# Kernel optimization log

Measured on AMD Instinct MI355X. Metric: run time of the kernel, lower is better.

## Reference

```python
import jax, jax.numpy as jnp
import numpy as np

N = 50000   # nodes
E = 400000  # edges
IN = 64     # input feature dim
H = 4       # heads (layers 1-2)
C = 128     # hidden channels per head
NEG_SLOPE = 0.2


def gat_conv(x, W, a_src, a_dst, b, src, dst, num_nodes):
    """PyG-style GATConv (add_self_loops=False, dropout inactive / eval mode).
    x: [N, F_in]; W: [F_in, H*C]; a_src/a_dst: [H, C]; b: [H*C].
    Returns concat-over-heads output [N, H*C]."""
    h = (x @ W).reshape(num_nodes, a_src.shape[0], a_src.shape[1])  # [N,H,C]
    alpha_s = jnp.einsum('nhc,hc->nh', h, a_src)  # [N,H]
    alpha_d = jnp.einsum('nhc,hc->nh', h, a_dst)  # [N,H]
    e = jax.nn.leaky_relu(alpha_s[src] + alpha_d[dst], NEG_SLOPE)  # [E,H]
    # numerically-stable segment softmax over incoming edges of each dst node
    m = jax.ops.segment_max(e, dst, num_segments=num_nodes)       # [N,H]
    m = jnp.where(jnp.isfinite(m), m, 0.0)                        # empty segments
    p = jnp.exp(e - m[dst])                                       # [E,H]
    denom = jax.ops.segment_sum(p, dst, num_segments=num_nodes)   # [N,H]
    alpha = p / (denom[dst] + 1e-16)                              # [E,H]
    # message = alpha * h[src], scatter-add into dst
    out = jax.ops.segment_sum(alpha[:, :, None] * h[src], dst,
                              num_segments=num_nodes)             # [N,H,C]
    return out.reshape(num_nodes, -1) + b


def setup_inputs() -> dict:
    key = jax.random.key(0)
    ks = jax.random.split(key, 16)
    s = 0.1  # weight scale for stability
    inp = {
        'x': jax.random.normal(ks[0], (N, IN), dtype=jnp.float32),
        'edge_index': jax.random.randint(ks[1], (2, E), 0, N, dtype=jnp.int64),
        # layer 1: 64 -> H*C
        'W1': s * jax.random.normal(ks[2], (IN, H * C), dtype=jnp.float32),
        'a_src1': s * jax.random.normal(ks[3], (H, C), dtype=jnp.float32),
        'a_dst1': s * jax.random.normal(ks[4], (H, C), dtype=jnp.float32),
        'b1': jnp.zeros((H * C,), dtype=jnp.float32),
        # layer 2: H*C -> H*C
        'W2': s * jax.random.normal(ks[5], (H * C, H * C), dtype=jnp.float32),
        'a_src2': s * jax.random.normal(ks[6], (H, C), dtype=jnp.float32),
        'a_dst2': s * jax.random.normal(ks[7], (H, C), dtype=jnp.float32),
        'b2': jnp.zeros((H * C,), dtype=jnp.float32),
        # layer 3: H*C -> C (heads=1)
        'W3': s * jax.random.normal(ks[8], (H * C, C), dtype=jnp.float32),
        'a_src3': s * jax.random.normal(ks[9], (1, C), dtype=jnp.float32),
        'a_dst3': s * jax.random.normal(ks[10], (1, C), dtype=jnp.float32),
        'b3': jnp.zeros((C,), dtype=jnp.float32),
    }
    return inp


def reference(x, edge_index, W1, a_src1, a_dst1, b1, W2, a_src2, a_dst2, b2,
              W3, a_src3, a_dst3, b3):
    src, dst = edge_index[0], edge_index[1]
    h = jax.nn.elu(gat_conv(x, W1, a_src1, a_dst1, b1, src, dst, N))
    h = jax.nn.elu(gat_conv(h, W2, a_src2, a_dst2, b2, src, dst, N))
    h = jax.nn.elu(gat_conv(h, W3, a_src3, a_dst3, b3, src, dst, N))
    return h  # [N, C]
```

## Files before the change

### kernel.cpp

```cpp
#include <hip/hip_runtime.h>
#include <math.h>


#define LRELU_SLOPE 0.2f
#define MPAD 50048

typedef __attribute__((ext_vector_type(8))) short short8;
typedef __attribute__((ext_vector_type(4))) float f32x4;

__device__ __forceinline__ float bf2f(unsigned int u) {
    return __uint_as_float(u << 16);
}
__device__ __forceinline__ unsigned short f2bf(float f) {
    unsigned int u = __float_as_uint(f);
    unsigned int r = u + 0x7FFFu + ((u >> 16) & 1u);
    return (unsigned short)(r >> 16);
}
__device__ __forceinline__ void load16_to_lds(const void* g, void* l) {
    __builtin_amdgcn_global_load_lds(
        (const __attribute__((address_space(1))) void*)g,
        (__attribute__((address_space(3))) void*)l, 16, 0, 0);
}
__device__ __forceinline__ float lrelu(float e) {
    return e > 0.f ? e : LRELU_SLOPE * e;
}


__global__ __launch_bounds__(256) void prep_kernel(
    const float* __restrict__ x, const float* __restrict__ W1,
    const float* __restrict__ W2, const float* __restrict__ W3,
    const float* __restrict__ as1, const float* __restrict__ ad1,
    unsigned short* __restrict__ x_bf, unsigned short* __restrict__ W1t,
    unsigned short* __restrict__ W2t, unsigned short* __restrict__ W3t,
    int* __restrict__ counts, float* __restrict__ ws, int N)
{
    int i = blockIdx.x * 256 + threadIdx.x;
    const int nx = N * 64;
    if (i < nx) { x_bf[i] = f2bf(x[i]); return; }
    i -= nx;
    if (i < 64 * 512) {
        int k = i / 512, nn = i % 512;
        W1t[nn * 64 + k] = f2bf(W1[i]);
        return;
    }
    i -= 64 * 512;
    if (i < 512 * 512) {
        int k = i / 512, nn = i % 512;
        W2t[nn * 512 + k] = f2bf(W2[i]);
        return;
    }
    i -= 512 * 512;
    if (i < 512 * 128) {
        int k = i / 128, nn = i % 128;
        W3t[(size_t)nn * 512 + k] = f2bf(W3[i]);
        return;
    }
    i -= 512 * 128;
    if (i < N) { counts[i] = 0; return; }
    i -= N;
    if (i < 256) {
        int h = i >> 6, k = i & 63;
        float ss = 0.f, sd = 0.f;
        for (int c = 0; c < 128; ++c) {
            float wv = W1[k * 512 + h * 128 + c];
            ss += wv * as1[h * 128 + c];
            sd += wv * ad1[h * 128 + c];
        }
        ws[i] = ss;
        ws[256 + i] = sd;
    }
}


__global__ void count_deg_kernel(const int* __restrict__ dst, int* __restrict__ counts, int E) {
    int e = blockIdx.x * blockDim.x + threadIdx.x;
    if (e < E) atomicAdd(&counts[dst[e]], 1);
}

__global__ __launch_bounds__(1024) void scan1_kernel(const int* __restrict__ counts,
                                                     int* __restrict__ row_ptr,
                                                     int* __restrict__ partial, int n) {
    __shared__ int wsum[16];
    const int t = threadIdx.x;
    const int lane = t & 63, w = t >> 6;
    const int i = blockIdx.x * 1024 + t;
    int v = (i < n) ? counts[i] : 0;
    int s = v;
    #pragma unroll
    for (int off = 1; off < 64; off <<= 1) {
        int u = __shfl_up(s, off);
        if (lane >= off) s += u;
    }
    if (lane == 63) wsum[w] = s;
    __syncthreads();
    if (w == 0 && lane < 16) {
        int tv = wsum[lane];
        #pragma unroll
        for (int off = 1; off < 16; off <<= 1) {
            int u = __shfl_up(tv, off);
            if (lane >= off) tv += u;
        }
        wsum[lane] = tv;
    }
    __syncthreads();
    int incl = s + (w > 0 ? wsum[w - 1] : 0);
    if (i < n) row_ptr[i + 1] = incl;
    if (t == 0) partial[blockIdx.x] = wsum[15];
}

__global__ void scan2_kernel(int* __restrict__ partial, int nb) {
    int lane = threadIdx.x;
    int v = (lane < nb) ? partial[lane] : 0;
    int s = v;
    #pragma unroll
    for (int off = 1; off < 64; off <<= 1) {
        int u = __shfl_up(s, off);
        if (lane >= off) s += u;
    }
    if (lane < nb) partial[lane] = s - v;
}

__global__ __launch_bounds__(1024) void scan3c_kernel(int* __restrict__ row_ptr,
                                                      const int* __restrict__ partial,
                                                      const int* __restrict__ counts,
                                                      int* __restrict__ cursor, int n) {
    const int i = blockIdx.x * 1024 + threadIdx.x;
    if (i < n) {
        int rp1 = row_ptr[i + 1] + partial[blockIdx.x];
        row_ptr[i + 1] = rp1;
        cursor[i] = rp1 - counts[i];
    }
    if (i == 0) row_ptr[0] = 0;
}

__global__ void fill_csr_kernel(const int* __restrict__ src, const int* __restrict__ dst,
                                int* __restrict__ cursor, int* __restrict__ csr_src, int E) {
    int e = blockIdx.x * blockDim.x + threadIdx.x;
    if (e < E) {
        int d = dst[e];
        int pos = atomicAdd(&cursor[d], 1);
        csr_src[pos] = src[e];
    }
}


__global__ __launch_bounds__(256) void als1_kernel(const float* __restrict__ x,
                                                   const float* __restrict__ ws,
                                                   float* __restrict__ als,
                                                   float* __restrict__ ald, int n_nodes) {
    const int lane = threadIdx.x & 63;
    const int wv = threadIdx.x >> 6;
    const int n = blockIdx.x * 4 + wv;
    if (n >= n_nodes) return;
    const float xv = x[(size_t)n * 64 + lane];
    float d0 = xv * ws[lane],        d1 = xv * ws[64 + lane];
    float d2 = xv * ws[128 + lane],  d3 = xv * ws[192 + lane];
    float e0 = xv * ws[256 + lane],  e1 = xv * ws[320 + lane];
    float e2 = xv * ws[384 + lane],  e3 = xv * ws[448 + lane];
    #pragma unroll
    for (int off = 32; off >= 1; off >>= 1) {
        d0 += __shfl_xor(d0, off); d1 += __shfl_xor(d1, off);
        d2 += __shfl_xor(d2, off); d3 += __shfl_xor(d3, off);
        e0 += __shfl_xor(e0, off); e1 += __shfl_xor(e1, off);
        e2 += __shfl_xor(e2, off); e3 += __shfl_xor(e3, off);
    }
    if (lane == 0) {
        float4 a = {d0, d1, d2, d3};
        float4 b = {e0, e1, e2, e3};
        *(float4*)&als[(size_t)n * 4] = a;
        *(float4*)&ald[(size_t)n * 4] = b;
    }
}


__global__ __launch_bounds__(256) void gatherx_kernel(
    const unsigned short* __restrict__ x_bf,
    const float* __restrict__ als, const float* __restrict__ ald,
    const int* __restrict__ row_ptr, const int* __restrict__ csr_src,
    unsigned short* __restrict__ xagg,
    int n_nodes)
{
    const int lane = threadIdx.x & 63;
    const int wv = threadIdx.x >> 6;
    const int n = blockIdx.x * 4 + wv;
    if (n >= n_nodes) return;
    const int head = lane >> 4;
    const int li = lane & 15;
    const int grpBase = lane & ~15;

    const int start = row_ptr[n];
    const int deg = row_ptr[n + 1] - start;
    const float aldv = ald[(size_t)n * 4 + head];

    float acc[4] = {};
    float wsum = 0.f;
    for (int base = 0; base < deg; base += 16) {
        const int cnt = min(16, deg - base);
        int s_l = 0; float w_l = 0.f;
        if (li < cnt) {
            s_l = csr_src[start + base + li];
            w_l = __expf(lrelu(als[(size_t)s_l * 4 + head] + aldv));
            wsum += w_l;
        }
        int sP = __shfl(s_l, grpBase);
        float aP = __shfl(w_l, grpBase);
        uint2 vP = *(const uint2*)(x_bf + (size_t)sP * 64 + li * 4);
        for (int e = 0; e < cnt; ++e) {
            const int nidx = (e + 1 < cnt) ? e + 1 : e;
            const int sN = __shfl(s_l, grpBase + nidx);
            const float aN = __shfl(w_l, grpBase + nidx);
            uint2 vN = *(const uint2*)(x_bf + (size_t)sN * 64 + li * 4);
            acc[0] += aP * bf2f(vP.x & 0xFFFFu);
            acc[1] += aP * bf2f(vP.x >> 16);
            acc[2] += aP * bf2f(vP.y & 0xFFFFu);
            acc[3] += aP * bf2f(vP.y >> 16);
            vP = vN; aP = aN;
        }
    }

    #pragma unroll
    for (int off = 8; off >= 1; off >>= 1) wsum += __shfl_xor(wsum, off);
    const float sc = (deg > 0) ? 1.f / wsum : 0.f;

    uint2 o;
    o.x = (unsigned int)f2bf(acc[0] * sc) | ((unsigned int)f2bf(acc[1] * sc) << 16);
    o.y = (unsigned int)f2bf(acc[2] * sc) | ((unsigned int)f2bf(acc[3] * sc) << 16);
    *(uint2*)&xagg[(size_t)n * 256 + head * 64 + li * 4] = o;
}


__global__ __launch_bounds__(256) void gemm_out_kernel(
    const unsigned short* __restrict__ A,
    const unsigned short* __restrict__ Bt,
    const float* __restrict__ bias,
    unsigned short* __restrict__ Cout,
    int M)
{
    __shared__ short As[2 * 128 * 32];
    __shared__ short Bs[2 * 128 * 32];
    const int t = threadIdx.x;
    const int w = t >> 6, lane = t & 63;
    const int wr = w >> 1, wc = w & 1;

    const int nwg = gridDim.x * gridDim.y;
    const int wg  = blockIdx.x + gridDim.x * blockIdx.y;
    const int qch = nwg >> 3, rch = nwg & 7;
    const int xcd = wg & 7, pos = wg >> 3;
    const int lg  = (xcd < rch ? xcd * (qch + 1) : rch * (qch + 1) + (xcd - rch) * qch) + pos;
    const int bx  = lg % gridDim.x;
    const int by  = lg / gridDim.x;

    const int rowBase = by * 128;
    const int head = bx;
    const int colBase = bx * 128;
    const int q = lane >> 4;
    const int r16 = lane & 15;
    const int qs = (q ^ ((r16 >> 1) & 3)) * 8;

    f32x4 acc[4][4] = {};

    const int sRow = t >> 2;
    const int sOff = ((t & 3) ^ ((sRow >> 1) & 3)) * 8;

    auto stage = [&](int kt, int b) {
        const int koff = kt * 32 + sOff;
        #pragma unroll
        for (int rr = 0; rr < 2; ++rr) {
            const unsigned short* gA = A + (size_t)(rowBase + rr * 64 + sRow) * 256 + head * 64 + koff;
            load16_to_lds(gA, (char*)As + b * 8192 + rr * 4096 + w * 1024);
            const unsigned short* gB = Bt + (size_t)(colBase + rr * 64 + sRow) * 64 + koff;
            load16_to_lds(gB, (char*)Bs + b * 8192 + rr * 4096 + w * 1024);
        }
    };

    stage(0, 0);
    __syncthreads();

    #pragma unroll
    for (int kt = 0; kt < 2; ++kt) {
        const int cur = kt & 1;
        if (kt + 1 < 2) stage(kt + 1, cur ^ 1);

        const short* Ab = As + cur * 4096;
        const short* Bb = Bs + cur * 4096;
        short8 af[4], bfr[4];
        #pragma unroll
        for (int m = 0; m < 4; ++m)
            af[m] = *(const short8*)&Ab[(wr * 64 + m * 16 + r16) * 32 + qs];
        #pragma unroll
        for (int n = 0; n < 4; ++n)
            bfr[n] = *(const short8*)&Bb[(wc * 64 + n * 16 + r16) * 32 + qs];
        #pragma unroll
        for (int m = 0; m < 4; ++m)
            #pragma unroll
            for (int n = 0; n < 4; ++n)
                acc[m][n] = __builtin_amdgcn_mfma_f32_16x16x32_bf16(af[m], bfr[n], acc[m][n], 0, 0, 0);

        __syncthreads();
    }

    float bv[4];
    #pragma unroll
    for (int n = 0; n < 4; ++n) bv[n] = bias[colBase + wc * 64 + n * 16 + r16];

    #pragma unroll
    for (int m = 0; m < 4; ++m) {
        #pragma unroll
        for (int r = 0; r < 4; ++r) {
            const int gr = rowBase + wr * 64 + m * 16 + q * 4 + r;
            if (gr < M) {
                #pragma unroll
                for (int n = 0; n < 4; ++n) {
                    float o = acc[m][n][r] + bv[n];
                    o = o > 0.f ? o : expm1f(o);
                    Cout[(size_t)gr * 512 + colBase + wc * 64 + n * 16 + r16] = f2bf(o);
                }
            }
        }
    }
}


__global__ __launch_bounds__(256) void gemm_mfma_kernel(
    const unsigned short* __restrict__ A,
    const unsigned short* __restrict__ Bt,
    unsigned short* __restrict__ C,
    const float* __restrict__ a_src,
    const float* __restrict__ a_dst,
    float* __restrict__ als,
    float* __restrict__ ald,
    int M, int N, int K, int H)
{
    __shared__ short As[2 * 128 * 32];
    __shared__ short Bs[2 * 128 * 32];
    const int t = threadIdx.x;
    const int w = t >> 6, lane = t & 63;
    const int wr = w >> 1, wc = w & 1;

    const int nwg = gridDim.x * gridDim.y;
    const int wg  = blockIdx.x + gridDim.x * blockIdx.y;
    const int qch = nwg >> 3, rch = nwg & 7;
    const int xcd = wg & 7, pos = wg >> 3;
    const int lg  = (xcd < rch ? xcd * (qch + 1) : rch * (qch + 1) + (xcd - rch) * qch) + pos;
    const int bx  = lg % gridDim.x;
    const int by  = lg / gridDim.x;

    const int rowBase = by * 128;
    const int colBase = bx * 128;
    const int q = lane >> 4;
    const int r16 = lane & 15;
    const int qs = (q ^ ((r16 >> 1) & 3)) * 8;

    f32x4 acc[4][4] = {};

    const int sRow = t >> 2;
    const int sOff = ((t & 3) ^ ((sRow >> 1) & 3)) * 8;

    const int NT = K >> 5;
    auto stage = [&](int kt, int b) {
        const int koff = kt * 32 + sOff;
        #pragma unroll
        for (int rr = 0; rr < 2; ++rr) {
            const unsigned short* gA = A + (size_t)(rowBase + rr * 64 + sRow) * K + koff;
            load16_to_lds(gA, (char*)As + b * 8192 + rr * 4096 + w * 1024);
            const unsigned short* gB = Bt + (size_t)(colBase + rr * 64 + sRow) * K + koff;
            load16_to_lds(gB, (char*)Bs + b * 8192 + rr * 4096 + w * 1024);
        }
    };

    stage(0, 0);
    __syncthreads();

    for (int kt = 0; kt < NT; ++kt) {
        const int cur = kt & 1;
        if (kt + 1 < NT) stage(kt + 1, cur ^ 1);

        const short* Ab = As + cur * 4096;
        const short* Bb = Bs + cur * 4096;
        short8 af[4], bfr[4];
        #pragma unroll
        for (int m = 0; m < 4; ++m)
            af[m] = *(const short8*)&Ab[(wr * 64 + m * 16 + r16) * 32 + qs];
        #pragma unroll
        for (int n = 0; n < 4; ++n)
            bfr[n] = *(const short8*)&Bb[(wc * 64 + n * 16 + r16) * 32 + qs];
        #pragma unroll
        for (int m = 0; m < 4; ++m)
            #pragma unroll
            for (int n = 0; n < 4; ++n)
                acc[m][n] = __builtin_amdgcn_mfma_f32_16x16x32_bf16(af[m], bfr[n], acc[m][n], 0, 0, 0);

        __syncthreads();
    }

    float asv[4], adv[4];
    #pragma unroll
    for (int n = 0; n < 4; ++n) {
        int col = colBase + wc * 64 + n * 16 + r16;
        asv[n] = a_src[col];
        adv[n] = a_dst[col];
    }
    const int head = bx;

    float* red = (float*)As;

    #pragma unroll
    for (int m = 0; m < 4; ++m) {
        #pragma unroll
        for (int r = 0; r < 4; ++r) {
            const int rowl = wr * 64 + m * 16 + q * 4 + r;
            const int gr = rowBase + rowl;
            float ps = 0.f, pd = 0.f;
            #pragma unroll
            for (int n = 0; n < 4; ++n) {
                ps += acc[m][n][r] * asv[n];
                pd += acc[m][n][r] * adv[n];
            }
            #pragma unroll
            for (int off = 8; off >= 1; off >>= 1) {
                ps += __shfl_xor(ps, off);
                pd += __shfl_xor(pd, off);
            }
            if (r16 == 0) {
                red[wc * 128 + rowl] = ps;
                red[256 + wc * 128 + rowl] = pd;
            }
            if (gr < M) {
                #pragma unroll
                for (int n = 0; n < 4; ++n)
                    C[(size_t)gr * N + colBase + wc * 64 + n * 16 + r16] = f2bf(acc[m][n][r]);
            }
        }
    }
    __syncthreads();
    if (t < 128) {
        const int gr = rowBase + t;
        if (gr < M) {
            als[(size_t)gr * H + head] = red[t] + red[128 + t];
            ald[(size_t)gr * H + head] = red[256 + t] + red[384 + t];
        }
    }
}


__global__ __launch_bounds__(256) void gather4f_kernel(
    const unsigned short* __restrict__ hfeat,
    const float* __restrict__ als, const float* __restrict__ ald,
    const int* __restrict__ row_ptr, const int* __restrict__ csr_src,
    const float* __restrict__ bias, unsigned short* __restrict__ out,
    int n_nodes)
{
    const int lane = threadIdx.x & 63;
    const int wv = threadIdx.x >> 6;
    const int n = blockIdx.x * 4 + wv;
    if (n >= n_nodes) return;
    const int head = lane >> 4;
    const int li = lane & 15;
    const int grpBase = lane & ~15;

    const int start = row_ptr[n];
    const int deg = row_ptr[n + 1] - start;
    const float aldv = ald[(size_t)n * 4 + head];

    float acc[8] = {};
    float wsum = 0.f;
    for (int base = 0; base < deg; base += 16) {
        const int cnt = min(16, deg - base);
        int s_l = 0; float w_l = 0.f;
        if (li < cnt) {
            s_l = csr_src[start + base + li];
            float e = als[(size_t)s_l * 4 + head] + aldv;
            w_l = __expf(lrelu(e));
            wsum += w_l;
        }
        int sP = __shfl(s_l, grpBase);
        float aP = __shfl(w_l, grpBase);
        short8 vP = *(const short8*)(hfeat + (size_t)sP * 512 + lane * 8);
        for (int e = 0; e < cnt; ++e) {
            const int nidx = (e + 1 < cnt) ? e + 1 : e;
            const int sN = __shfl(s_l, grpBase + nidx);
            const float aN = __shfl(w_l, grpBase + nidx);
            short8 vN = *(const short8*)(hfeat + (size_t)sN * 512 + lane * 8);
            #pragma unroll
            for (int j = 0; j < 8; ++j)
                acc[j] += aP * bf2f((unsigned int)(unsigned short)vP[j]);
            vP = vN; aP = aN;
        }
    }

    #pragma unroll
    for (int off = 8; off >= 1; off >>= 1) wsum += __shfl_xor(wsum, off);
    const float sc = (deg > 0) ? 1.f / wsum : 0.f;

    float ov[8];
    #pragma unroll
    for (int j = 0; j < 8; ++j) {
        float o = acc[j] * sc + bias[lane * 8 + j];
        ov[j] = o > 0.f ? o : expm1f(o);
    }
    short8 v;
    #pragma unroll
    for (int j = 0; j < 8; ++j) v[j] = (short)f2bf(ov[j]);
    *(short8*)&out[(size_t)n * 512 + lane * 8] = v;
}


__global__ __launch_bounds__(256) void gather1f_kernel(
    const unsigned short* __restrict__ hfeat,
    const float* __restrict__ als, const float* __restrict__ ald,
    const int* __restrict__ row_ptr, const int* __restrict__ csr_src,
    const float* __restrict__ bias, float* __restrict__ out, int n_nodes)
{
    const int lane = threadIdx.x & 63;
    const int wv = threadIdx.x >> 6;
    const int n = blockIdx.x * 4 + wv;
    if (n >= n_nodes) return;
    const int qid = lane >> 4;
    const int ql = lane & 15;

    const int start = row_ptr[n];
    const int deg = row_ptr[n + 1] - start;
    const float aldv = ald[n];

    float acc[8] = {};
    float wsum = 0.f;
    for (int base = 0; base < deg; base += 64) {
        const int cnt = min(64, deg - base);
        int s_l = 0; float w_l = 0.f;
        if (lane < cnt) {
            s_l = csr_src[start + base + lane];
            float e = als[s_l] + aldv;
            w_l = __expf(lrelu(e));
            wsum += w_l;
        }
        int idx = qid;
        int idxc = idx < cnt ? idx : 0;
        int sP = __shfl(s_l, idxc);
        float awP = __shfl(w_l, idxc);
        float aP = idx < cnt ? awP : 0.f;
        short8 vP = *(const short8*)(hfeat + (size_t)sP * 128 + ql * 8);
        for (int e = 0; e < cnt; e += 4) {
            const int nidxRaw = e + 4 + qid;
            const int nidxc = nidxRaw < cnt ? nidxRaw : 0;
            const int sN = __shfl(s_l, nidxc);
            const float awN = __shfl(w_l, nidxc);
            const float aN = nidxRaw < cnt ? awN : 0.f;
            short8 vN = *(const short8*)(hfeat + (size_t)sN * 128 + ql * 8);
            #pragma unroll
            for (int j = 0; j < 8; ++j)
                acc[j] += aP * bf2f((unsigned int)(unsigned short)vP[j]);
            vP = vN; aP = aN;
        }
    }

    #pragma unroll
    for (int off = 32; off >= 1; off >>= 1) wsum += __shfl_xor(wsum, off);
    const float sc = (deg > 0) ? 1.f / wsum : 0.f;

    #pragma unroll
    for (int j = 0; j < 8; ++j) {
        acc[j] += __shfl_xor(acc[j], 16);
        acc[j] += __shfl_xor(acc[j], 32);
    }

    if (qid == 0) {
        float tmp[8];
        #pragma unroll
        for (int j = 0; j < 8; ++j) {
            float o = acc[j] * sc + bias[ql * 8 + j];
            tmp[j] = o > 0.f ? o : expm1f(o);
        }
        float4 o0 = {tmp[0], tmp[1], tmp[2], tmp[3]};
        float4 o1 = {tmp[4], tmp[5], tmp[6], tmp[7]};
        float* op = out + (size_t)n * 128 + ql * 8;
        *(float4*)op = o0;
        *(float4*)(op + 4) = o1;
    }
}


extern "C" void kernel_launch(void* const* d_in, const int* in_sizes, int n_in,
                              void* d_out, int out_size, void* d_ws, size_t ws_size,
                              hipStream_t stream) {
    const float* x   = (const float*)d_in[0];
    const int*   ei  = (const int*)d_in[1];
    const float* W1  = (const float*)d_in[2];
    const float* as1 = (const float*)d_in[3];
    const float* ad1 = (const float*)d_in[4];
    const float* b1  = (const float*)d_in[5];
    const float* W2  = (const float*)d_in[6];
    const float* as2 = (const float*)d_in[7];
    const float* ad2 = (const float*)d_in[8];
    const float* b2  = (const float*)d_in[9];
    const float* W3  = (const float*)d_in[10];
    const float* as3 = (const float*)d_in[11];
    const float* ad3 = (const float*)d_in[12];
    const float* b3  = (const float*)d_in[13];

    const int N = in_sizes[0] / 64;
    const int E = in_sizes[1] / 2;
    const int HC = 512;

    const int* src = ei;
    const int* dst = ei + E;

    size_t off = 0;
    auto carve = [&](size_t bytes) -> void* {
        void* p = (char*)d_ws + off;
        off += (bytes + 255) & ~(size_t)255;
        return p;
    };
    unsigned short* x_bf    = (unsigned short*)carve((size_t)MPAD * 64 * 2);
    unsigned short* feat_bf = (unsigned short*)carve((size_t)MPAD * HC * 2);
    unsigned short* h_bf    = (unsigned short*)carve((size_t)N * HC * 2);
    unsigned short* xagg    = (unsigned short*)carve((size_t)MPAD * 256 * 2);
    unsigned short* W1t     = (unsigned short*)carve((size_t)512 * 64 * 2);
    unsigned short* W2t     = (unsigned short*)carve((size_t)512 * 512 * 2);
    unsigned short* W3t     = (unsigned short*)carve((size_t)128 * 512 * 2);
    float* stats  = (float*)carve((size_t)N * 8 * sizeof(float));
    float* als    = stats;
    float* ald    = stats + (size_t)N * 4;
    float* ws     = (float*)carve(512 * sizeof(float) * 2);
    int*   counts = (int*)carve((size_t)N * sizeof(int));
    int*   row_ptr= (int*)carve((size_t)(N + 1) * sizeof(int));
    int*   cursor = (int*)carve((size_t)N * sizeof(int));
    int*   csr_src= (int*)carve((size_t)E * sizeof(int));
    int*   partial= (int*)carve(64 * sizeof(int));
    (void)ws_size;

    const int nb = (N + 1023) / 1024;
    const int prepTotal = N * 64 + 64 * 512 + 512 * 512 + 512 * 128 + N + 256;

    prep_kernel<<<(prepTotal + 255) / 256, 256, 0, stream>>>(
        x, W1, W2, W3, as1, ad1, x_bf, W1t, W2t, W3t, counts, ws, N);

    count_deg_kernel<<<(E + 255) / 256, 256, 0, stream>>>(dst, counts, E);
    scan1_kernel<<<nb, 1024, 0, stream>>>(counts, row_ptr, partial, N);
    scan2_kernel<<<1, 64, 0, stream>>>(partial, nb);
    scan3c_kernel<<<nb, 1024, 0, stream>>>(row_ptr, partial, counts, cursor, N);
    fill_csr_kernel<<<(E + 255) / 256, 256, 0, stream>>>(src, dst, cursor, csr_src, E);

    const int rowTiles = (N + 127) / 128;
    const int aggBlocks = (N + 3) / 4;

    als1_kernel<<<aggBlocks, 256, 0, stream>>>(x, ws, als, ald, N);
    gatherx_kernel<<<aggBlocks, 256, 0, stream>>>(x_bf, als, ald, row_ptr, csr_src, xagg, N);
    gemm_out_kernel<<<dim3(4, rowTiles), 256, 0, stream>>>(xagg, W1t, b1, feat_bf, N);

    gemm_mfma_kernel<<<dim3(4, rowTiles), 256, 0, stream>>>(feat_bf, W2t, h_bf, as2, ad2,
                                                            als, ald, N, 512, 512, 4);
    gather4f_kernel<<<aggBlocks, 256, 0, stream>>>(h_bf, als, ald, row_ptr, csr_src,
                                                   b2, feat_bf, N);

    gemm_mfma_kernel<<<dim3(1, rowTiles), 256, 0, stream>>>(feat_bf, W3t, h_bf, as3, ad3,
                                                            als, ald, N, 128, 512, 1);
    gather1f_kernel<<<aggBlocks, 256, 0, stream>>>(h_bf, als, ald, row_ptr, csr_src,
                                                   b3, (float*)d_out, N);
}
```

Measured before the change: 351.7 us.

## Remap gatherx lanes to process eight edges concurrently across all heads

Result: slower. 380.8 us (+8.3%).

```diff
diff --git a/kernel.cpp b/kernel.cpp
--- a/kernel.cpp
+++ b/kernel.cpp
@@ -184,48 +184,76 @@
     const int wv = threadIdx.x >> 6;
     const int n = blockIdx.x * 4 + wv;
     if (n >= n_nodes) return;
-    const int head = lane >> 4;
-    const int li = lane & 15;
-    const int grpBase = lane & ~15;
+    const int g = lane >> 3;
+    const int j = lane & 7;
 
     const int start = row_ptr[n];
     const int deg = row_ptr[n + 1] - start;
-    const float aldv = ald[(size_t)n * 4 + head];
-
-    float acc[4] = {};
-    float wsum = 0.f;
-    for (int base = 0; base < deg; base += 16) {
-        const int cnt = min(16, deg - base);
-        int s_l = 0; float w_l = 0.f;
-        if (li < cnt) {
-            s_l = csr_src[start + base + li];
-            w_l = __expf(lrelu(als[(size_t)s_l * 4 + head] + aldv));
-            wsum += w_l;
-        }
-        int sP = __shfl(s_l, grpBase);
-        float aP = __shfl(w_l, grpBase);
-        uint2 vP = *(const uint2*)(x_bf + (size_t)sP * 64 + li * 4);
-        for (int e = 0; e < cnt; ++e) {
-            const int nidx = (e + 1 < cnt) ? e + 1 : e;
-            const int sN = __shfl(s_l, grpBase + nidx);
-            const float aN = __shfl(w_l, grpBase + nidx);
-            uint2 vN = *(const uint2*)(x_bf + (size_t)sN * 64 + li * 4);
-            acc[0] += aP * bf2f(vP.x & 0xFFFFu);
-            acc[1] += aP * bf2f(vP.x >> 16);
-            acc[2] += aP * bf2f(vP.y & 0xFFFFu);
-            acc[3] += aP * bf2f(vP.y >> 16);
-            vP = vN; aP = aN;
-        }
-    }
-
-    #pragma unroll
-    for (int off = 8; off >= 1; off >>= 1) wsum += __shfl_xor(wsum, off);
-    const float sc = (deg > 0) ? 1.f / wsum : 0.f;
-
-    uint2 o;
-    o.x = (unsigned int)f2bf(acc[0] * sc) | ((unsigned int)f2bf(acc[1] * sc) << 16);
-    o.y = (unsigned int)f2bf(acc[2] * sc) | ((unsigned int)f2bf(acc[3] * sc) << 16);
-    *(uint2*)&xagg[(size_t)n * 256 + head * 64 + li * 4] = o;
+    const float4 aldv = *(const float4*)&ald[(size_t)n * 4];
+
+    float acc[4][8] = {};
+    float wsx = 0.f, wsy = 0.f, wsz = 0.f, wsw = 0.f;
+
+    for (int base = 0; base < deg; base += 8) {
+        const int cnt = min(8, deg - base);
+        int s_l = 0;
+        float ax_l = 0.f, ay_l = 0.f, az_l = 0.f, aw_l = 0.f;
+        if (lane < cnt) {
+            s_l = csr_src[start + base + lane];
+            float4 a = *(const float4*)&als[(size_t)s_l * 4];
+            ax_l = __expf(lrelu(a.x + aldv.x));
+            ay_l = __expf(lrelu(a.y + aldv.y));
+            az_l = __expf(lrelu(a.z + aldv.z));
+            aw_l = __expf(lrelu(a.w + aldv.w));
+            wsx += ax_l; wsy += ay_l; wsz += az_l; wsw += aw_l;
+        }
+        const int sg  = __shfl(s_l, g);
+        const float a0 = __shfl(ax_l, g);
+        const float a1 = __shfl(ay_l, g);
+        const float a2 = __shfl(az_l, g);
+        const float a3 = __shfl(aw_l, g);
+        short8 v = *(const short8*)(x_bf + (size_t)sg * 64 + j * 8);
+        #pragma unroll
+        for (int c = 0; c < 8; ++c) {
+            const float xv = bf2f((unsigned int)(unsigned short)v[c]);
+            acc[0][c] += a0 * xv;
+            acc[1][c] += a1 * xv;
+            acc[2][c] += a2 * xv;
+            acc[3][c] += a3 * xv;
+        }
+    }
+
+    #pragma unroll
+    for (int off = 1; off < 64; off <<= 1) {
+        wsx += __shfl_xor(wsx, off);
+        wsy += __shfl_xor(wsy, off);
+        wsz += __shfl_xor(wsz, off);
+        wsw += __shfl_xor(wsw, off);
+    }
+    float sc[4];
+    sc[0] = deg > 0 ? 1.f / wsx : 0.f;
+    sc[1] = deg > 0 ? 1.f / wsy : 0.f;
+    sc[2] = deg > 0 ? 1.f / wsz : 0.f;
+    sc[3] = deg > 0 ? 1.f / wsw : 0.f;
+
+    #pragma unroll
+    for (int h = 0; h < 4; ++h)
+        #pragma unroll
+        for (int c = 0; c < 8; ++c) {
+            acc[h][c] += __shfl_xor(acc[h][c], 8);
+            acc[h][c] += __shfl_xor(acc[h][c], 16);
+            acc[h][c] += __shfl_xor(acc[h][c], 32);
+        }
+
+    if (g == 0) {
+        #pragma unroll
+        for (int h = 0; h < 4; ++h) {
+            short8 o;
+            #pragma unroll
+            for (int c = 0; c < 8; ++c) o[c] = (short)f2bf(acc[h][c] * sc[h]);
+            *(short8*)&xagg[(size_t)n * 256 + h * 64 + j * 8] = o;
+        }
+    }
 }
 
 
```
